# Kernel optimization log

Measured on AMD Instinct MI355X. Metric: run time of the kernel, lower is better.

## Reference

```python
import jax, jax.numpy as jnp
import numpy as np

D_MODEL = 1024
N_LAYER = 4
VOCAB = 50288  # 50277 padded to multiple of 16
D_STATE = 128
D_CONV = 4
HEADDIM = 64
CHUNK = 64
D_INNER = 2 * D_MODEL            # expand=2 -> 2048
NHEADS = D_INNER // HEADDIM      # 32
D_IN_PROJ = 2 * D_INNER + 2 * D_STATE + NHEADS  # ngroups=1
CONV_DIM = D_INNER + 2 * D_STATE
BATCH = 1
SEQLEN = 1024
EPS = 1e-5


def silu(x):
    return x * jax.nn.sigmoid(x)


def rmsnorm(x, w, z=None):
    if z is not None:
        x = x * silu(z)
    return x * jax.lax.rsqrt(jnp.mean(x * x, axis=-1, keepdims=True) + EPS) * w


def segsum(x):
    # x: (..., T) -> (..., T, T) with segment sums below diagonal, -inf above
    T = x.shape[-1]
    xe = jnp.broadcast_to(x[..., None], x.shape + (T,))
    mask_lo = jnp.tril(jnp.ones((T, T), dtype=bool), -1)
    xe = jnp.where(mask_lo, xe, 0.0)
    s = jnp.cumsum(xe, axis=-2)
    mask = jnp.tril(jnp.ones((T, T), dtype=bool), 0)
    return jnp.where(mask, s, -jnp.inf)


def ssd(x, dt, A, B, C, Dp):
    # x: (b,s,h,p), dt/A-broadcast: (b,s,h), B/C: (b,s,n) (ngroups=1), Dp: (h,)
    b, s = x.shape[0], x.shape[1]
    nchunks = s // CHUNK
    xD = x * Dp[:, None]
    Adt = A * dt                      # (b,s,h)
    xdt = x * dt[..., None]
    xr = xdt.reshape(b, nchunks, CHUNK, NHEADS, HEADDIM)
    Ar = Adt.reshape(b, nchunks, CHUNK, NHEADS).transpose(0, 3, 1, 2)  # (b,h,c,l)
    Br = B.reshape(b, nchunks, CHUNK, D_STATE)
    Cr = C.reshape(b, nchunks, CHUNK, D_STATE)
    A_cumsum = jnp.cumsum(Ar, axis=-1)                  # (b,h,c,l)
    L = jnp.exp(segsum(Ar))                             # (b,h,c,l,l)
    Y_diag = jnp.einsum('bcln,bcsn,bhcls,bcshp->bclhp', Cr, Br, L, xr)
    decay_states = jnp.exp(A_cumsum[..., -1:] - A_cumsum)
    states = jnp.einsum('bcln,bhcl,bclhp->bchpn', Br, decay_states, xr)
    states = jnp.concatenate([jnp.zeros_like(states[:, :1]), states], axis=1)
    decay_chunk = jnp.exp(segsum(jnp.pad(A_cumsum[..., -1], ((0, 0), (0, 0), (1, 0)))))
    new_states = jnp.einsum('bhzc,bchpn->bzhpn', decay_chunk, states)
    states = new_states[:, :-1]
    state_decay_out = jnp.exp(A_cumsum)
    Y_off = jnp.einsum('bcln,bchpn,bhcl->bclhp', Cr, states, state_decay_out)
    Y = (Y_diag + Y_off).reshape(b, s, NHEADS, HEADDIM) + xD
    return Y


def mamba2_forward(input_ids, embedding, norm_w, in_proj_w, conv_w, conv_b,
                   dt_bias, A_log, D, mixer_norm_w, out_proj_w, norm_f_w):
    h = embedding[input_ids]  # (b,s,d_model)
    for l in range(N_LAYER):
        u = rmsnorm(h, norm_w[l])
        zxbcdt = u @ in_proj_w[l].T  # (b,s,d_in_proj)
        z = zxbcdt[..., :D_INNER]
        xBC = zxbcdt[..., D_INNER:D_INNER + CONV_DIM]
        dt = jax.nn.softplus(zxbcdt[..., -NHEADS:] + dt_bias[l])
        # causal depthwise conv1d
        xc = jnp.transpose(xBC, (0, 2, 1))
        xc = jax.lax.conv_general_dilated(
            xc, conv_w[l], (1,), [(D_CONV - 1, 0)],
            dimension_numbers=('NCH', 'OIH', 'NCH'),
            feature_group_count=CONV_DIM) + conv_b[l][None, :, None]
        xBC = silu(jnp.transpose(xc, (0, 2, 1)))
        x = xBC[..., :D_INNER].reshape(BATCH, SEQLEN, NHEADS, HEADDIM)
        B = xBC[..., D_INNER:D_INNER + D_STATE]
        C = xBC[..., D_INNER + D_STATE:]
        A = -jnp.exp(A_log[l])  # (h,)
        y = ssd(x, dt, A, B, C, D[l])
        y = rmsnorm(y.reshape(BATCH, SEQLEN, D_INNER), mixer_norm_w[l], z)
        h = h + y @ out_proj_w[l].T
    h = rmsnorm(h, norm_f_w)
    return h @ embedding.T  # tied lm_head


def setup_inputs() -> dict:
    key = jax.random.key(0)
    ks = jax.random.split(key, 10)
    def rn(k, shape, s=0.02):
        return jax.random.normal(k, shape, jnp.float32) * s
    return {
        'input_ids': jax.random.randint(ks[0], (BATCH, SEQLEN), 0, VOCAB, jnp.int32),
        'embedding': rn(ks[1], (VOCAB, D_MODEL)),
        'norm_w': jnp.ones((N_LAYER, D_MODEL), jnp.float32),
        'in_proj_w': rn(ks[2], (N_LAYER, D_IN_PROJ, D_MODEL)),
        'conv_w': rn(ks[3], (N_LAYER, CONV_DIM, 1, D_CONV), 0.2),
        'conv_b': jnp.zeros((N_LAYER, CONV_DIM), jnp.float32),
        'dt_bias': rn(ks[4], (N_LAYER, NHEADS), 0.5),
        'A_log': jnp.log(jax.random.uniform(ks[5], (N_LAYER, NHEADS), jnp.float32, 1.0, 16.0)),
        'D': jnp.ones((N_LAYER, NHEADS), jnp.float32) + rn(ks[6], (N_LAYER, NHEADS), 0.1),
        'mixer_norm_w': jnp.ones((N_LAYER, D_INNER), jnp.float32),
        'out_proj_w': rn(ks[7], (N_LAYER, D_MODEL, D_INNER)),
        'norm_f_w': jnp.ones((D_MODEL,), jnp.float32),
    }


def reference(input_ids, embedding, norm_w, in_proj_w, conv_w, conv_b,
              dt_bias, A_log, D, mixer_norm_w, out_proj_w, norm_f_w):
    return mamba2_forward(input_ids, embedding, norm_w, in_proj_w, conv_w, conv_b,
                          dt_bias, A_log, D, mixer_norm_w, out_proj_w, norm_f_w)
```

## Files before the change

kernel.cpp:

```cpp
#include <hip/hip_runtime.h>
#include <hip/hip_bf16.h>
#include <math.h>

#define D_MODEL   1024
#define VOCAB     50288
#define D_STATE   128
#define D_CONV    4
#define HEADDIM   64
#define CHUNK     64
#define D_INNER   2048
#define NHEADS    32
#define D_IN_PROJ 4384
#define CONV_DIM  2304
#define SEQ       1024
#define NCHUNKS   16
#define EPS       1e-5f
#define SZH       1048576

typedef __bf16 bf16x8 __attribute__((ext_vector_type(8)));
typedef __bf16 bf16x4 __attribute__((ext_vector_type(4)));
typedef float  f32x4  __attribute__((ext_vector_type(4)));

__device__ __forceinline__ float blockReduceSum256(float v, float* sm) {
    #pragma unroll
    for (int off = 32; off > 0; off >>= 1) v += __shfl_down(v, off);
    if ((threadIdx.x & 63) == 0) sm[threadIdx.x >> 6] = v;
    __syncthreads();
    return sm[0] + sm[1] + sm[2] + sm[3];
}

__device__ __forceinline__ float sigmoidf_(float x) { return 1.0f / (1.0f + expf(-x)); }

__device__ __forceinline__ void gload_lds16(const __bf16* g, __bf16* l) {
    __builtin_amdgcn_global_load_lds(
        (const __attribute__((address_space(1))) void*)g,
        (__attribute__((address_space(3))) void*)l,
        16, 0, 0);
}

__global__ void cvt_bf16_k(const float* __restrict__ src, __bf16* __restrict__ dst, long n) {
    long i = ((long)blockIdx.x * 256 + threadIdx.x) * 8;
    long stride = (long)gridDim.x * 256 * 8;
    for (; i < n; i += stride) {
        float4 a = *(const float4*)(src + i);
        float4 b = *(const float4*)(src + i + 4);
        bf16x8 o;
        o[0] = (__bf16)a.x; o[1] = (__bf16)a.y; o[2] = (__bf16)a.z; o[3] = (__bf16)a.w;
        o[4] = (__bf16)b.x; o[5] = (__bf16)b.y; o[6] = (__bf16)b.z; o[7] = (__bf16)b.w;
        *(bf16x8*)(dst + i) = o;
    }
}

__global__ void gather_k(const int* __restrict__ ids, const float* __restrict__ emb,
                         float* __restrict__ h) {
    int s = blockIdx.x;
    int id = ids[s];
    const float4* src = (const float4*)(emb + (size_t)id * D_MODEL);
    float4* dst = (float4*)(h + (size_t)s * D_MODEL);
    dst[threadIdx.x] = src[threadIdx.x];
}

__global__ void rmsnorm_k(const float* __restrict__ x, const float* __restrict__ w,
                          float* __restrict__ o) {
    __shared__ float red[4];
    int s = blockIdx.x, t = threadIdx.x;
    float4 v = ((const float4*)(x + (size_t)s * D_MODEL))[t];
    float ss = v.x*v.x + v.y*v.y + v.z*v.z + v.w*v.w;
    float tot = blockReduceSum256(ss, red);
    float r = rsqrtf(tot / (float)D_MODEL + EPS);
    float4 wv = ((const float4*)w)[t];
    float4 ov;
    ov.x = v.x * r * wv.x; ov.y = v.y * r * wv.y;
    ov.z = v.z * r * wv.z; ov.w = v.w * r * wv.w;
    ((float4*)(o + (size_t)s * D_MODEL))[t] = ov;
}

__global__ void rmsnorm_fold_bf16_k(float* __restrict__ h, const float* __restrict__ o,
                                    const float* __restrict__ w, __bf16* __restrict__ out) {
    __shared__ float red[4];
    int s = blockIdx.x, t = threadIdx.x;
    float4 v = ((const float4*)(h + (size_t)s * D_MODEL))[t];
    if (o) {
        #pragma unroll
        for (int j = 0; j < 4; ++j) {
            float4 ov = ((const float4*)(o + (size_t)j * SZH + (size_t)s * D_MODEL))[t];
            v.x += ov.x; v.y += ov.y; v.z += ov.z; v.w += ov.w;
        }
        ((float4*)(h + (size_t)s * D_MODEL))[t] = v;
    }
    float ss = v.x*v.x + v.y*v.y + v.z*v.z + v.w*v.w;
    float tot = blockReduceSum256(ss, red);
    float r = rsqrtf(tot / (float)D_MODEL + EPS);
    float4 wv = ((const float4*)w)[t];
    bf16x4 ov;
    ov[0] = (__bf16)(v.x * r * wv.x); ov[1] = (__bf16)(v.y * r * wv.y);
    ov[2] = (__bf16)(v.z * r * wv.z); ov[3] = (__bf16)(v.w * r * wv.w);
    *(bf16x4*)(out + (size_t)s * D_MODEL + t * 4) = ov;
}

__global__ void gatednorm_k(float* __restrict__ Y, const float* __restrict__ zx,
                            const float* __restrict__ w) {
    __shared__ float red[4];
    int s = blockIdx.x, t = threadIdx.x;
    float4 y0 = ((const float4*)(Y + (size_t)s * D_INNER))[2*t];
    float4 y1 = ((const float4*)(Y + (size_t)s * D_INNER))[2*t+1];
    float4 z0 = ((const float4*)(zx + (size_t)s * D_IN_PROJ))[2*t];
    float4 z1 = ((const float4*)(zx + (size_t)s * D_IN_PROJ))[2*t+1];
    float g[8];
    float yv[8] = { y0.x,y0.y,y0.z,y0.w, y1.x,y1.y,y1.z,y1.w };
    float zv[8] = { z0.x,z0.y,z0.z,z0.w, z1.x,z1.y,z1.z,z1.w };
    float ss = 0.f;
    #pragma unroll
    for (int j = 0; j < 8; ++j) {
        float gg = yv[j] * zv[j] * sigmoidf_(zv[j]);
        g[j] = gg;
        ss += gg * gg;
    }
    float tot = blockReduceSum256(ss, red);
    float r = rsqrtf(tot / (float)D_INNER + EPS);
    float4 o0, o1;
    o0.x = g[0]*r*w[8*t+0]; o0.y = g[1]*r*w[8*t+1]; o0.z = g[2]*r*w[8*t+2]; o0.w = g[3]*r*w[8*t+3];
    o1.x = g[4]*r*w[8*t+4]; o1.y = g[5]*r*w[8*t+5]; o1.z = g[6]*r*w[8*t+6]; o1.w = g[7]*r*w[8*t+7];
    ((float4*)(Y + (size_t)s * D_INNER))[2*t]   = o0;
    ((float4*)(Y + (size_t)s * D_INNER))[2*t+1] = o1;
}

__global__ void gatednorm_bf16_k(const float* __restrict__ Y, const float* __restrict__ zx0,
                                 const float* __restrict__ zx1,
                                 const float* __restrict__ w, __bf16* __restrict__ o) {
    __shared__ float red[4];
    int s = blockIdx.x, t = threadIdx.x;
    float4 y0 = ((const float4*)(Y + (size_t)s * D_INNER))[2*t];
    float4 y1 = ((const float4*)(Y + (size_t)s * D_INNER))[2*t+1];
    float4 z0 = ((const float4*)(zx0 + (size_t)s * D_IN_PROJ))[2*t];
    float4 z1 = ((const float4*)(zx0 + (size_t)s * D_IN_PROJ))[2*t+1];
    if (zx1) {
        float4 a0 = ((const float4*)(zx1 + (size_t)s * D_IN_PROJ))[2*t];
        float4 a1 = ((const float4*)(zx1 + (size_t)s * D_IN_PROJ))[2*t+1];
        z0.x += a0.x; z0.y += a0.y; z0.z += a0.z; z0.w += a0.w;
        z1.x += a1.x; z1.y += a1.y; z1.z += a1.z; z1.w += a1.w;
    }
    float g[8];
    float yv[8] = { y0.x,y0.y,y0.z,y0.w, y1.x,y1.y,y1.z,y1.w };
    float zv[8] = { z0.x,z0.y,z0.z,z0.w, z1.x,z1.y,z1.z,z1.w };
    float ss = 0.f;
    #pragma unroll
    for (int j = 0; j < 8; ++j) {
        float gg = yv[j] * zv[j] * sigmoidf_(zv[j]);
        g[j] = gg;
        ss += gg * gg;
    }
    float tot = blockReduceSum256(ss, red);
    float r = rsqrtf(tot / (float)D_INNER + EPS);
    bf16x8 ov;
    #pragma unroll
    for (int j = 0; j < 8; ++j) ov[j] = (__bf16)(g[j] * r * w[8*t+j]);
    *(bf16x8*)(o + (size_t)s * D_INNER + t * 8) = ov;
}

__global__ __launch_bounds__(512) void gemm256_8ph(const __bf16* __restrict__ A,
                                                   const __bf16* __restrict__ B,
                                                   float* __restrict__ C,
                                                   int N, int K,
                                                   int lda, int ldb, int ldc,
                                                   int ntiles) {
    extern __shared__ __bf16 lds[];

    const int d = blockIdx.x;
    const int xcd = d & 7, kk = d >> 3;
    const int m_tile = kk & 3, p = kk >> 2;
    const int n_tile = xcd + (p << 3);
    if (n_tile >= ntiles) return;
    const int bm0 = m_tile * 256, bn0 = n_tile * 256;

    const int tid = threadIdx.x;
    const int l = tid & 63, w = tid >> 6;
    const int wr = w >> 2, wc = w & 3;
    const int lrow = l & 15;
    const int kb8 = (((l >> 4) ^ ((l >> 1) & 3)) << 3);
    const int srow_off = (w << 4) + (l >> 2);
    const int sk8 = (((l & 3) ^ ((l >> 3) & 3)) << 3);

    f32x4 acc[8][4];
    #pragma unroll
    for (int m = 0; m < 8; ++m)
        #pragma unroll
        for (int n = 0; n < 4; ++n) acc[m][n] = (f32x4){0.f,0.f,0.f,0.f};

    auto stage = [&](int kt, int b) {
        __bf16* base = lds + b * 16384;
        #pragma unroll
        for (int r = 0; r < 2; ++r) {
            int row = r * 128 + srow_off;
            const __bf16* g = A + (size_t)(bm0 + row) * lda + kt * 32 + sk8;
            gload_lds16(g, base + r * 4096 + w * 512);
        }
        #pragma unroll
        for (int r = 0; r < 2; ++r) {
            int row = r * 128 + srow_off;
            int grn = bn0 + row; if (grn > N - 1) grn = N - 1;
            const __bf16* g = B + (size_t)grn * ldb + kt * 32 + sk8;
            gload_lds16(g, base + 8192 + r * 4096 + w * 512);
        }
    };

    stage(0, 0);
    stage(1, 1);
    asm volatile("s_waitcnt vmcnt(4)" ::: "memory");
    __builtin_amdgcn_s_barrier();

    const int nt = K / 32;
    for (int t = 0; t < nt; ++t) {
        const int b = t & 1;
        const int bb = b * 16384;
        bf16x8 af[4], bfv[4];
        #pragma unroll
        for (int m = 0; m < 4; ++m)
            af[m] = *(const bf16x8*)&lds[bb + (wr * 128 + m * 16 + lrow) * 32 + kb8];
        #pragma unroll
        for (int n = 0; n < 4; ++n)
            bfv[n] = *(const bf16x8*)&lds[bb + 8192 + (wc * 64 + n * 16 + lrow) * 32 + kb8];
        __builtin_amdgcn_s_barrier();
        __builtin_amdgcn_s_setprio(1);
        #pragma unroll
        for (int m = 0; m < 4; ++m)
            #pragma unroll
            for (int n = 0; n < 4; ++n)
                acc[m][n] = __builtin_amdgcn_mfma_f32_16x16x32_bf16(af[m], bfv[n], acc[m][n], 0, 0, 0);
        __builtin_amdgcn_s_setprio(0);
        __builtin_amdgcn_s_barrier();
        #pragma unroll
        for (int m = 0; m < 4; ++m)
            af[m] = *(const bf16x8*)&lds[bb + (wr * 128 + (m + 4) * 16 + lrow) * 32 + kb8];
        __builtin_amdgcn_s_barrier();
        __builtin_amdgcn_s_setprio(1);
        #pragma unroll
        for (int m = 0; m < 4; ++m)
            #pragma unroll
            for (int n = 0; n < 4; ++n)
                acc[m + 4][n] = __builtin_amdgcn_mfma_f32_16x16x32_bf16(af[m], bfv[n], acc[m + 4][n], 0, 0, 0);
        __builtin_amdgcn_s_setprio(0);
        __builtin_amdgcn_s_barrier();
        asm volatile("" ::: "memory");
        if (t + 2 < nt) {
            stage(t + 2, b);
            asm volatile("s_waitcnt vmcnt(4)" ::: "memory");
            __builtin_amdgcn_s_barrier();
        } else if (t + 1 < nt) {
            asm volatile("s_waitcnt vmcnt(0)" ::: "memory");
            __builtin_amdgcn_s_barrier();
        }
    }

    const int r0q = (l >> 4) * 4;
    #pragma unroll
    for (int m = 0; m < 8; ++m) {
        int gr = bm0 + wr * 128 + m * 16 + r0q;
        #pragma unroll
        for (int n = 0; n < 4; ++n) {
            int gc = bn0 + wc * 64 + n * 16 + lrow;
            if (gc < N) {
                #pragma unroll
                for (int rr = 0; rr < 4; ++rr)
                    C[(size_t)(gr + rr) * ldc + gc] = acc[m][n][rr];
            }
        }
    }
}

template<int TM, int TN, int MTL2, bool ACC>
__global__ __launch_bounds__(256) void gemm_bt_bf16(const __bf16* __restrict__ A,
                                                    const __bf16* __restrict__ B,
                                                    float* __restrict__ C,
                                                    int N, int klen,
                                                    int lda, int ldb, int ldc,
                                                    int ntiles, size_t csplit) {
    constexpr int FM = TM / 32;
    constexpr int FN = TN / 32;
    __shared__ __bf16 As[TM * 32];
    __shared__ __bf16 Bs[TN * 32];

    const int d = blockIdx.x;
    const int xcd = d & 7;
    const int kk = d >> 3;
    const int p = kk >> MTL2;
    const int m_tile = kk & ((1 << MTL2) - 1);
    const int n_tile = xcd + (p << 3);
    if (n_tile >= ntiles) return;

    const int k_begin = blockIdx.y * klen;
    C += (size_t)blockIdx.y * csplit;

    const int bm0 = m_tile * TM;
    const int bn0 = n_tile * TN;
    const int t = threadIdx.x;
    const int l = t & 63;
    const int w = t >> 6;
    const int wr = w >> 1, wc = w & 1;
    const int lrow = l & 15;
    const int lk   = (l >> 4) * 8;
    const int srow = l >> 2;
    const int scol = (l & 3) * 8;

    f32x4 acc[FM][FN];
    #pragma unroll
    for (int m = 0; m < FM; ++m)
        #pragma unroll
        for (int n = 0; n < FN; ++n)
            acc[m][n] = (f32x4){0.f, 0.f, 0.f, 0.f};

    for (int k0 = k_begin; k0 < k_begin + klen; k0 += 32) {
        __syncthreads();
        #pragma unroll
        for (int i = 0; i < TM / 64; ++i) {
            int r0 = w * (TM / 4) + i * 16;
            const __bf16* g = A + (size_t)(bm0 + r0 + srow) * lda + k0 + scol;
            gload_lds16(g, As + (size_t)r0 * 32);
        }
        #pragma unroll
        for (int i = 0; i < TN / 64; ++i) {
            int r0 = w * (TN / 4) + i * 16;
            int gn = bn0 + r0 + srow; if (gn > N - 1) gn = N - 1;
            const __bf16* g = B + (size_t)gn * ldb + k0 + scol;
            gload_lds16(g, Bs + (size_t)r0 * 32);
        }
        __syncthreads();

        bf16x8 af[FM], bfr[FN];
        #pragma unroll
        for (int m = 0; m < FM; ++m)
            af[m] = *(const bf16x8*)&As[(wr * (TM/2) + m * 16 + lrow) * 32 + lk];
        #pragma unroll
        for (int n = 0; n < FN; ++n)
            bfr[n] = *(const bf16x8*)&Bs[(wc * (TN/2) + n * 16 + lrow) * 32 + lk];
        #pragma unroll
        for (int m = 0; m < FM; ++m)
            #pragma unroll
            for (int n = 0; n < FN; ++n)
                acc[m][n] = __builtin_amdgcn_mfma_f32_16x16x32_bf16(af[m], bfr[n], acc[m][n], 0, 0, 0);
    }

    const int r0 = (l >> 4) * 4;
    #pragma unroll
    for (int m = 0; m < FM; ++m) {
        #pragma unroll
        for (int rr = 0; rr < 4; ++rr) {
            int gr = bm0 + wr * (TM/2) + m * 16 + r0 + rr;
            #pragma unroll
            for (int n = 0; n < FN; ++n) {
                int gc = bn0 + wc * (TN/2) + n * 16 + lrow;
                if (gc < N) {
                    size_t off = (size_t)gr * ldc + gc;
                    if (ACC) C[off] += acc[m][n][rr];
                    else     C[off]  = acc[m][n][rr];
                }
            }
        }
    }
}

template<bool ACC>
__global__ __launch_bounds__(256) void gemm_nt_cvt(const float* __restrict__ A,
                                                   const float* __restrict__ B,
                                                   float* __restrict__ C,
                                                   int M, int N, int K,
                                                   int lda, int ldb, int ldc) {
    __shared__ __bf16 As[128][40];
    __shared__ __bf16 Bs[128][40];
    const int bm0 = blockIdx.x * 128;
    const int bn0 = blockIdx.y * 128;
    const int t = threadIdx.x;
    const int l = t & 63;
    const int w = t >> 6;
    const int wr = w >> 1;
    const int wc = w & 1;
    const int lrow = l & 15;
    const int lk   = (l >> 4) * 8;

    f32x4 acc[4][4];
    #pragma unroll
    for (int m = 0; m < 4; ++m)
        #pragma unroll
        for (int n = 0; n < 4; ++n)
            acc[m][n] = (f32x4){0.f, 0.f, 0.f, 0.f};

    for (int k0 = 0; k0 < K; k0 += 32) {
        __syncthreads();
        float4 av[4], bv[4];
        #pragma unroll
        for (int i = 0; i < 4; ++i) {
            int idx = t + i * 256;
            int r = idx >> 3;
            int c4 = (idx & 7) * 4;
            av[i] = *(const float4*)(A + (size_t)(bm0 + r) * lda + k0 + c4);
            int gn = bn0 + r; if (gn > N - 1) gn = N - 1;
            bv[i] = *(const float4*)(B + (size_t)gn * ldb + k0 + c4);
        }
        #pragma unroll
        for (int i = 0; i < 4; ++i) {
            int idx = t + i * 256;
            int r = idx >> 3;
            int c4 = (idx & 7) * 4;
            bf16x4 aw, bw;
            aw[0] = (__bf16)av[i].x; aw[1] = (__bf16)av[i].y;
            aw[2] = (__bf16)av[i].z; aw[3] = (__bf16)av[i].w;
            bw[0] = (__bf16)bv[i].x; bw[1] = (__bf16)bv[i].y;
            bw[2] = (__bf16)bv[i].z; bw[3] = (__bf16)bv[i].w;
            *(bf16x4*)&As[r][c4] = aw;
            *(bf16x4*)&Bs[r][c4] = bw;
        }
        __syncthreads();

        bf16x8 af[4], bfr[4];
        #pragma unroll
        for (int m = 0; m < 4; ++m)
            af[m] = *(const bf16x8*)&As[wr * 64 + m * 16 + lrow][lk];
        #pragma unroll
        for (int n = 0; n < 4; ++n)
            bfr[n] = *(const bf16x8*)&Bs[wc * 64 + n * 16 + lrow][lk];
        #pragma unroll
        for (int m = 0; m < 4; ++m)
            #pragma unroll
            for (int n = 0; n < 4; ++n)
                acc[m][n] = __builtin_amdgcn_mfma_f32_16x16x32_bf16(af[m], bfr[n], acc[m][n], 0, 0, 0);
    }

    const int r0 = (l >> 4) * 4;
    #pragma unroll
    for (int m = 0; m < 4; ++m) {
        #pragma unroll
        for (int rr = 0; rr < 4; ++rr) {
            int gr = bm0 + wr * 64 + m * 16 + r0 + rr;
            #pragma unroll
            for (int n = 0; n < 4; ++n) {
                int gc = bn0 + wc * 64 + n * 16 + lrow;
                if (gc < N) {
                    size_t off = (size_t)gr * ldc + gc;
                    if (ACC) C[off] += acc[m][n][rr];
                    else     C[off]  = acc[m][n][rr];
                }
            }
        }
    }
}

__global__ void conv_silu_k(const float* __restrict__ zx0, const float* __restrict__ zx1,
                            const float* __restrict__ w,
                            const float* __restrict__ b, float* __restrict__ xBC) {
    int idx = blockIdx.x * 256 + threadIdx.x;
    if (idx >= SEQ * CONV_DIM) return;
    int s = idx / CONV_DIM, c = idx - s * CONV_DIM;
    float acc = b[c];
    #pragma unroll
    for (int k = 0; k < D_CONV; ++k) {
        int si = s + k - (D_CONV - 1);
        if (si >= 0) {
            size_t o = (size_t)si * D_IN_PROJ + D_INNER + c;
            float v = zx0[o];
            if (zx1) v += zx1[o];
            acc = fmaf(v, w[c * D_CONV + k], acc);
        }
    }
    xBC[idx] = acc * sigmoidf_(acc);
}

__global__ void dtcum_k(const float* __restrict__ zx0, const float* __restrict__ zx1,
                        const float* __restrict__ dt_bias,
                        const float* __restrict__ A_log,
                        float* __restrict__ dtb, float* __restrict__ acs) {
    int c = blockIdx.x, h = blockIdx.y, l = threadIdx.x;
    int s = c * 64 + l;
    size_t o = (size_t)s * D_IN_PROJ + (D_IN_PROJ - NHEADS) + h;
    float v = zx0[o];
    if (zx1) v += zx1[o];
    v += dt_bias[h];
    float dt = (v > 20.f) ? v : log1pf(expf(v));
    dtb[(size_t)s * NHEADS + h] = dt;
    float a = -expf(A_log[h]);
    float x = a * dt;
    #pragma unroll
    for (int off = 1; off < 64; off <<= 1) {
        float oo = __shfl_up(x, off);
        if (l >= off) x += oo;
    }
    acs[(size_t)h * SEQ + s] = x;
}

__global__ __launch_bounds__(256) void cmg_k(const float* __restrict__ xBC,
                                             float* __restrict__ cm,
                                             __bf16* __restrict__ btg) {
    const int c = blockIdx.x;
    const int LDP = 136;
    __shared__ __bf16 Cs[64 * 136];
    __shared__ __bf16 Bs[64 * 136];
    const int t = threadIdx.x;
    const int l = t & 63;
    const int w = t >> 6;

    #pragma unroll
    for (int i = 0; i < 8; ++i) {
        int e = t + i * 256;
        int row = e >> 5, n4 = (e & 31) * 4;
        float4 vc = *(const float4*)(xBC + (size_t)(c*64 + row) * CONV_DIM + D_INNER + D_STATE + n4);
        float4 vb = *(const float4*)(xBC + (size_t)(c*64 + row) * CONV_DIM + D_INNER + n4);
        bf16x4 cc, bb;
        cc[0] = (__bf16)vc.x; cc[1] = (__bf16)vc.y; cc[2] = (__bf16)vc.z; cc[3] = (__bf16)vc.w;
        bb[0] = (__bf16)vb.x; bb[1] = (__bf16)vb.y; bb[2] = (__bf16)vb.z; bb[3] = (__bf16)vb.w;
        *(bf16x4*)&Cs[row * LDP + n4] = cc;
        *(bf16x4*)&Bs[row * LDP + n4] = bb;
    }
    __syncthreads();

    #pragma unroll
    for (int i = 0; i < 4; ++i) {
        int e8 = t + i * 256;
        int n = e8 >> 3, l8 = (e8 & 7) * 8;
        bf16x8 o;
        #pragma unroll
        for (int j = 0; j < 8; ++j) o[j] = Bs[(l8 + j) * LDP + n];
        *(bf16x8*)(btg + ((size_t)c * 128 + n) * 64 + l8) = o;
    }

    const int lrow = l & 15;
    const int lk   = (l >> 4) * 8;
    const int l0 = w * 16;
    f32x4 acc[4];
    #pragma unroll
    for (int n = 0; n < 4; ++n) acc[n] = (f32x4){0.f,0.f,0.f,0.f};
    #pragma unroll
    for (int kc = 0; kc < 4; ++kc) {
        bf16x8 a = *(const bf16x8*)&Cs[(l0 + lrow) * LDP + kc * 32 + lk];
        #pragma unroll
        for (int n = 0; n < 4; ++n) {
            bf16x8 b = *(const bf16x8*)&Bs[(n * 16 + lrow) * LDP + kc * 32 + lk];
            acc[n] = __builtin_amdgcn_mfma_f32_16x16x32_bf16(a, b, acc[n], 0, 0, 0);
        }
    }
    const int r0 = (l >> 4) * 4;
    #pragma unroll
    for (int n = 0; n < 4; ++n)
        #pragma unroll
        for (int r = 0; r < 4; ++r)
            cm[(size_t)c * 4096 + (l0 + r0 + r) * 64 + n * 16 + lrow] = acc[n][r];
}

__global__ __launch_bounds__(256) void ydst_k(const float* __restrict__ cm,
                                              const __bf16* __restrict__ btg,
                                              const float* __restrict__ xBC,
                                              const float* __restrict__ dtb,
                                              const float* __restrict__ acs,
                                              float* __restrict__ Y,
                                              float* __restrict__ st) {
    const int c = blockIdx.x, h = blockIdx.y;
    const int LDP = 72;
    __shared__ __bf16 Xt[64 * 72];
    __shared__ __bf16 X2[64 * 72];
    __shared__ __bf16 G [64 * 72];
    __shared__ __bf16 Bt[128 * 72];
    __shared__ float arow[64];
    __shared__ float decl[64];
    const int t = threadIdx.x;
    const int l = t & 63;
    const int w = t >> 6;

    if (t < 64) arow[t] = acs[(size_t)h * SEQ + c * 64 + t];
    __syncthreads();
    const float alast = arow[63];
    if (t < 64) decl[t] = expf(alast - arow[t]);
    #pragma unroll
    for (int i = 0; i < 16; ++i) {
        int e = t + i * 256;
        int gl = e >> 6, sx = e & 63;
        G[gl * LDP + sx] = (sx <= gl) ? (__bf16)(cm[(size_t)c * 4096 + e] * expf(arow[gl] - arow[sx])) : (__bf16)0.f;
    }
    #pragma unroll
    for (int i = 0; i < 4; ++i) {
        int e8 = t + i * 256;
        int n = e8 >> 3, l8 = (e8 & 7) * 8;
        *(bf16x8*)&Bt[n * LDP + l8] = *(const bf16x8*)(btg + ((size_t)c * 128 + n) * 64 + l8);
    }
    __syncthreads();
    #pragma unroll
    for (int i = 0; i < 4; ++i) {
        int e4 = t + i * 256;
        int sx = e4 >> 4, p4 = (e4 & 15) * 4;
        int s = c * 64 + sx;
        float4 v = *(const float4*)(xBC + (size_t)s * CONV_DIM + h * HEADDIM + p4);
        float d = dtb[(size_t)s * NHEADS + h];
        float d2 = d * decl[sx];
        Xt[(p4+0) * LDP + sx] = (__bf16)(v.x * d);
        Xt[(p4+1) * LDP + sx] = (__bf16)(v.y * d);
        Xt[(p4+2) * LDP + sx] = (__bf16)(v.z * d);
        Xt[(p4+3) * LDP + sx] = (__bf16)(v.w * d);
        X2[(p4+0) * LDP + sx] = (__bf16)(v.x * d2);
        X2[(p4+1) * LDP + sx] = (__bf16)(v.y * d2);
        X2[(p4+2) * LDP + sx] = (__bf16)(v.z * d2);
        X2[(p4+3) * LDP + sx] = (__bf16)(v.w * d2);
    }
    __syncthreads();

    const int lrow = l & 15;
    const int lk   = (l >> 4) * 8;
    const int p0 = w * 16;
    const int r0 = (l >> 4) * 4;

    f32x4 acc1[4];
    #pragma unroll
    for (int n = 0; n < 4; ++n) acc1[n] = (f32x4){0.f,0.f,0.f,0.f};
    #pragma unroll
    for (int kc = 0; kc < 2; ++kc) {
        bf16x8 a = *(const bf16x8*)&Xt[(p0 + lrow) * LDP + kc * 32 + lk];
        #pragma unroll
        for (int n = 0; n < 4; ++n) {
            bf16x8 b = *(const bf16x8*)&G[(n * 16 + lrow) * LDP + kc * 32 + lk];
            acc1[n] = __builtin_amdgcn_mfma_f32_16x16x32_bf16(a, b, acc1[n], 0, 0, 0);
        }
    }
    #pragma unroll
    for (int n = 0; n < 4; ++n) {
        int lc = n * 16 + lrow;
        float4 ov; ov.x = acc1[n][0]; ov.y = acc1[n][1]; ov.z = acc1[n][2]; ov.w = acc1[n][3];
        *(float4*)(Y + (size_t)(c*64 + lc) * D_INNER + h * HEADDIM + p0 + r0) = ov;
    }

    f32x4 acc2[8];
    #pragma unroll
    for (int n = 0; n < 8; ++n) acc2[n] = (f32x4){0.f,0.f,0.f,0.f};
    #pragma unroll
    for (int kc = 0; kc < 2; ++kc) {
        bf16x8 a = *(const bf16x8*)&X2[(p0 + lrow) * LDP + kc * 32 + lk];
        #pragma unroll
        for (int n = 0; n < 8; ++n) {
            bf16x8 b = *(const bf16x8*)&Bt[(n * 16 + lrow) * LDP + kc * 32 + lk];
            acc2[n] = __builtin_amdgcn_mfma_f32_16x16x32_bf16(a, b, acc2[n], 0, 0, 0);
        }
    }
    float* stb = st + ((size_t)(c * NHEADS + h) * 64) * 128;
    #pragma unroll
    for (int n = 0; n < 8; ++n) {
        int nc = n * 16 + lrow;
        #pragma unroll
        for (int r = 0; r < 4; ++r)
            stb[(size_t)(p0 + r0 + r) * 128 + nc] = acc2[n][r];
    }
}

__global__ void rec_k(float* __restrict__ st, const float* __restrict__ acs) {
    int idx = blockIdx.x * 256 + threadIdx.x;
    int h = idx >> 13;
    float S = 0.f;
    for (int c = 0; c < NCHUNKS; ++c) {
        float* p = st + (size_t)c * (NHEADS * D_STATE * HEADDIM) + idx;
        float tmp = *p;
        *p = S;
        float dec = expf(acs[(size_t)h * SEQ + c * 64 + 63]);
        S = fmaf(S, dec, tmp);
    }
}

__global__ __launch_bounds__(256) void yoff_k(const float* __restrict__ xBC,
                                              const float* __restrict__ acs,
                                              const float* __restrict__ st,
                                              const float* __restrict__ Dp,
                                              float* __restrict__ Y) {
    const int c = blockIdx.x, h = blockIdx.y;
    const int LDP = 136;
    __shared__ __bf16 Sts[64 * 136];
    __shared__ __bf16 Cs [64 * 136];
    __shared__ float arow[64];
    const int t = threadIdx.x;
    const int l = t & 63;
    const int w = t >> 6;

    if (t < 64) arow[t] = acs[(size_t)h * SEQ + c * 64 + t];
    const float* stb = st + ((size_t)(c * NHEADS + h) * 64) * 128;
    #pragma unroll
    for (int i = 0; i < 8; ++i) {
        int e = t + i * 256;
        int row = e >> 5, n4 = (e & 31) * 4;
        float4 vs = *(const float4*)(stb + (size_t)row * 128 + n4);
        float4 vc = *(const float4*)(xBC + (size_t)(c*64 + row) * CONV_DIM + D_INNER + D_STATE + n4);
        bf16x4 ss, cc;
        ss[0] = (__bf16)vs.x; ss[1] = (__bf16)vs.y; ss[2] = (__bf16)vs.z; ss[3] = (__bf16)vs.w;
        cc[0] = (__bf16)vc.x; cc[1] = (__bf16)vc.y; cc[2] = (__bf16)vc.z; cc[3] = (__bf16)vc.w;
        *(bf16x4*)&Sts[row * LDP + n4] = ss;
        *(bf16x4*)&Cs [row * LDP + n4] = cc;
    }
    __syncthreads();

    const int lrow = l & 15;
    const int lk   = (l >> 4) * 8;
    const int p0 = w * 16;
    const int r0 = (l >> 4) * 4;
    const float dpar = Dp[h];

    f32x4 acc[4];
    #pragma unroll
    for (int n = 0; n < 4; ++n) acc[n] = (f32x4){0.f,0.f,0.f,0.f};
    #pragma unroll
    for (int kc = 0; kc < 4; ++kc) {
        bf16x8 a = *(const bf16x8*)&Sts[(p0 + lrow) * LDP + kc * 32 + lk];
        #pragma unroll
        for (int n = 0; n < 4; ++n) {
            bf16x8 b = *(const bf16x8*)&Cs[(n * 16 + lrow) * LDP + kc * 32 + lk];
            acc[n] = __builtin_amdgcn_mfma_f32_16x16x32_bf16(a, b, acc[n], 0, 0, 0);
        }
    }
    #pragma unroll
    for (int n = 0; n < 4; ++n) {
        int lc = n * 16 + lrow;
        int s = c * 64 + lc;
        float sc = expf(arow[lc]);
        float4 xv = *(const float4*)(xBC + (size_t)s * CONV_DIM + h * HEADDIM + p0 + r0);
        float4 yv = *(float4*)(Y + (size_t)s * D_INNER + h * HEADDIM + p0 + r0);
        yv.x += sc * acc[n][0] + dpar * xv.x;
        yv.y += sc * acc[n][1] + dpar * xv.y;
        yv.z += sc * acc[n][2] + dpar * xv.z;
        yv.w += sc * acc[n][3] + dpar * xv.w;
        *(float4*)(Y + (size_t)s * D_INNER + h * HEADDIM + p0 + r0) = yv;
    }
}

extern "C" void kernel_launch(void* const* d_in, const int* in_sizes, int n_in,
                              void* d_out, int out_size, void* d_ws, size_t ws_size,
                              hipStream_t stream) {
    const int*   ids          = (const int*)d_in[0];
    const float* emb          = (const float*)d_in[1];
    const float* norm_w       = (const float*)d_in[2];
    const float* in_proj_w    = (const float*)d_in[3];
    const float* conv_w       = (const float*)d_in[4];
    const float* conv_b       = (const float*)d_in[5];
    const float* dt_bias      = (const float*)d_in[6];
    const float* A_log        = (const float*)d_in[7];
    const float* Dp           = (const float*)d_in[8];
    const float* mixer_norm_w = (const float*)d_in[9];
    const float* out_proj_w   = (const float*)d_in[10];
    const float* norm_f_w     = (const float*)d_in[11];
    float* out = (float*)d_out;

    const size_t SZ_H = SZH, SZ_U = SZH, SZ_ZX = 4489216, SZ_XBC = 2359296,
                 SZ_DT = 32768, SZ_ACS = 32768, SZ_CM = 65536, SZ_ST = 4194304, SZ_Y = 2097152;
    const size_t SZ_BTG_F = 65536;
    const size_t BF_U = SZ_H, BF_Y = SZ_Y;
    const size_t BF_WIN  = 4ull * 4489216;
    const size_t BF_WOUT = 4ull * 2097152;
    const size_t BF_EMB  = (size_t)VOCAB * D_MODEL;

    const size_t f32_base = SZ_H + SZ_U + SZ_ZX + SZ_XBC + SZ_DT + SZ_ACS + SZ_CM + SZ_BTG_F + SZ_ST + SZ_Y;
    const size_t f32_new  = f32_base + SZ_ZX + 4 * SZ_H;
    const size_t bf_all   = (BF_U + BF_Y + BF_WIN + BF_WOUT + BF_EMB) * 2;
    const size_t bytesNew = f32_new * 4 + bf_all;
    const size_t bytesOld = f32_base * 4 + bf_all;
    const int tier = (ws_size >= bytesNew) ? 0 : (ws_size >= bytesOld) ? 1 : 2;

    float *h, *u, *dtb, *acs, *cm, *zx, *zxb = nullptr, *xBC, *st, *Y, *o = nullptr;
    __bf16 *btg, *ub = nullptr, *Yb = nullptr, *win = nullptr, *wout = nullptr, *embb = nullptr;

    if (tier <= 1) {
        float* f = (float*)d_ws;
        h = f;   f += SZ_H;
        u = f;   f += SZ_U;
        dtb = f; f += SZ_DT;
        acs = f; f += SZ_ACS;
        cm = f;  f += SZ_CM;
        btg = (__bf16*)f; f += SZ_BTG_F;
        zx = f;  f += SZ_ZX;
        if (tier == 0) {
            zxb = f; f += SZ_ZX;
            o = f;   f += 4 * SZ_H;
        }
        xBC = f; f += SZ_XBC;
        st = f;  f += SZ_ST;
        Y = f;   f += SZ_Y;
        __bf16* bb = (__bf16*)f;
        ub = bb;   bb += BF_U;
        Yb = bb;   bb += BF_Y;
        win = bb;  bb += BF_WIN;
        wout = bb; bb += BF_WOUT;
        embb = bb;
    } else {
        float* f = (float*)d_ws;
        h = f;   f += SZ_H;
        u = f;   f += SZ_U;
        dtb = f; f += SZ_DT;
        acs = f; f += SZ_ACS;
        cm = f;  f += SZ_CM;
        btg = (__bf16*)f; f += SZ_BTG_F;
        float* ob = (float*)d_out;
        zx = ob;
        xBC = zx + SZ_ZX;
        st = xBC + SZ_XBC;
        Y = st + SZ_ST;
    }

    if (tier <= 1) {
        cvt_bf16_k<<<(int)(BF_WIN / 2048), 256, 0, stream>>>(in_proj_w, win, (long)BF_WIN);
        cvt_bf16_k<<<(int)(BF_WOUT / 2048), 256, 0, stream>>>(out_proj_w, wout, (long)BF_WOUT);
        cvt_bf16_k<<<(int)(BF_EMB / 2048), 256, 0, stream>>>(emb, embb, (long)BF_EMB);
    }

    gather_k<<<SEQ, 256, 0, stream>>>(ids, emb, h);

    const int NT_IN  = (D_IN_PROJ + 127) / 128;
    const int NT_OUT = D_MODEL / 128;
    const int GX_IN  = 8 * ((NT_IN  + 7) / 8) * 8;
    const int GX_OUT = 8 * ((NT_OUT + 7) / 8) * 16;
    const int NT_LM256 = (VOCAB + 255) / 256;
    const int GX_LM256 = 8 * ((NT_LM256 + 7) / 8) * 4;

    for (int l = 0; l < 4; ++l) {
        if (tier <= 1) {
            rmsnorm_fold_bf16_k<<<SEQ, 256, 0, stream>>>(
                h, (tier == 0 && l > 0) ? o : nullptr, norm_w + (size_t)l * D_MODEL, ub);
            if (tier == 0) {
                gemm_bt_bf16<128, 128, 3, false><<<dim3(GX_IN, 2), 256, 0, stream>>>(
                    ub, win + (size_t)l * 4489216, zx,
                    D_IN_PROJ, 512, D_MODEL, D_MODEL, D_IN_PROJ, NT_IN, SZ_ZX);
            } else {
                gemm_bt_bf16<128, 128, 3, false><<<dim3(GX_IN, 1), 256, 0, stream>>>(
                    ub, win + (size_t)l * 4489216, zx,
                    D_IN_PROJ, 1024, D_MODEL, D_MODEL, D_IN_PROJ, NT_IN, 0);
            }
        } else {
            rmsnorm_k<<<SEQ, 256, 0, stream>>>(h, norm_w + (size_t)l * D_MODEL, u);
            gemm_nt_cvt<false><<<dim3(8, 35), 256, 0, stream>>>(
                u, in_proj_w + (size_t)l * D_IN_PROJ * D_MODEL, zx,
                SEQ, D_IN_PROJ, D_MODEL, D_MODEL, D_MODEL, D_IN_PROJ);
        }

        float* zx1 = (tier == 0) ? zxb : nullptr;

        conv_silu_k<<<(SEQ * CONV_DIM) / 256, 256, 0, stream>>>(
            zx, zx1, conv_w + (size_t)l * CONV_DIM * D_CONV, conv_b + (size_t)l * CONV_DIM, xBC);

        dtcum_k<<<dim3(NCHUNKS, NHEADS), 64, 0, stream>>>(
            zx, zx1, dt_bias + (size_t)l * NHEADS, A_log + (size_t)l * NHEADS, dtb, acs);

        cmg_k<<<NCHUNKS, 256, 0, stream>>>(xBC, cm, btg);

        ydst_k<<<dim3(NCHUNKS, NHEADS), 256, 0, stream>>>(cm, btg, xBC, dtb, acs, Y, st);

        rec_k<<<(NHEADS * D_STATE * HEADDIM) / 256, 256, 0, stream>>>(st, acs);

        yoff_k<<<dim3(NCHUNKS, NHEADS), 256, 0, stream>>>(xBC, acs, st, Dp + (size_t)l * NHEADS, Y);

        if (tier <= 1) {
            gatednorm_bf16_k<<<SEQ, 256, 0, stream>>>(Y, zx, zx1, mixer_norm_w + (size_t)l * D_INNER, Yb);
            if (tier == 0) {
                gemm_bt_bf16<64, 128, 4, false><<<dim3(GX_OUT, 4), 256, 0, stream>>>(
                    Yb, wout + (size_t)l * 2097152, o,
                    D_MODEL, 512, D_INNER, D_INNER, D_MODEL, NT_OUT, SZ_H);
            } else {
                gemm_bt_bf16<64, 128, 4, true><<<dim3(GX_OUT, 1), 256, 0, stream>>>(
                    Yb, wout + (size_t)l * 2097152, h,
                    D_MODEL, 2048, D_INNER, D_INNER, D_MODEL, NT_OUT, 0);
            }
        } else {
            gatednorm_k<<<SEQ, 256, 0, stream>>>(Y, zx, mixer_norm_w + (size_t)l * D_INNER);
            gemm_nt_cvt<true><<<dim3(8, 8), 256, 0, stream>>>(
                Y, out_proj_w + (size_t)l * D_MODEL * D_INNER, h,
                SEQ, D_MODEL, D_INNER, D_INNER, D_INNER, D_MODEL);
        }
    }

    if (tier <= 1) {
        rmsnorm_fold_bf16_k<<<SEQ, 256, 0, stream>>>(
            h, (tier == 0) ? o : nullptr, norm_f_w, ub);
        gemm256_8ph<<<dim3(GX_LM256), 512, 65536, stream>>>(
            ub, embb, out, VOCAB, 1024, D_MODEL, D_MODEL, VOCAB, NT_LM256);
    } else {
        rmsnorm_k<<<SEQ, 256, 0, stream>>>(h, norm_f_w, u);
        gemm_nt_cvt<false><<<dim3(8, (VOCAB + 127) / 128), 256, 0, stream>>>(
            u, emb, out, SEQ, VOCAB, D_MODEL, D_MODEL, D_MODEL, VOCAB);
    }
}
```

Measured before the change: 720.3 us.

## Deepen LM-head GEMM pipeline to four LDS stages with single-phase MFMA loop

Replaces the double-buffered two-phase LM-head GEMM with a four-buffer pipeline that prefetches three K-tiles ahead, using graded vmcnt waits and one barrier pair per iteration. All eight A fragments are loaded up front and the full 8x4 MFMA block is issued in a single burst, removing the interleaved half-tile barriers. The intent is to hide global-load latency better and cut synchronisation overhead. In exchange it uses 128 KB of static LDS and more VGPRs for fragments, which may reduce occupancy. It also drops the barrier between LDS fragment reads and the next stage write.

```diff
diff --git a/kernel.cpp b/kernel.cpp
--- a/kernel.cpp
+++ b/kernel.cpp
@@ -158,13 +158,13 @@
     *(bf16x8*)(o + (size_t)s * D_INNER + t * 8) = ov;
 }
 
-__global__ __launch_bounds__(512) void gemm256_8ph(const __bf16* __restrict__ A,
-                                                   const __bf16* __restrict__ B,
-                                                   float* __restrict__ C,
-                                                   int N, int K,
-                                                   int lda, int ldb, int ldc,
-                                                   int ntiles) {
-    extern __shared__ __bf16 lds[];
+__global__ __launch_bounds__(512) void gemm256_p4(const __bf16* __restrict__ A,
+                                                  const __bf16* __restrict__ B,
+                                                  float* __restrict__ C,
+                                                  int N, int K,
+                                                  int lda, int ldb, int ldc,
+                                                  int ntiles) {
+    __shared__ __bf16 lds[4 * 16384];
 
     const int d = blockIdx.x;
     const int xcd = d & 7, kk = d >> 3;
@@ -206,50 +206,34 @@
 
     stage(0, 0);
     stage(1, 1);
-    asm volatile("s_waitcnt vmcnt(4)" ::: "memory");
-    __builtin_amdgcn_s_barrier();
+    stage(2, 2);
 
     const int nt = K / 32;
     for (int t = 0; t < nt; ++t) {
-        const int b = t & 1;
-        const int bb = b * 16384;
-        bf16x8 af[4], bfv[4];
-        #pragma unroll
-        for (int m = 0; m < 4; ++m)
+        const int bb = (t & 3) * 16384;
+        if (t + 3 < nt) stage(t + 3, (t + 3) & 3);
+        if (t + 3 < nt)      asm volatile("s_waitcnt vmcnt(12)" ::: "memory");
+        else if (t + 2 < nt) asm volatile("s_waitcnt vmcnt(8)"  ::: "memory");
+        else if (t + 1 < nt) asm volatile("s_waitcnt vmcnt(4)"  ::: "memory");
+        else                 asm volatile("s_waitcnt vmcnt(0)"  ::: "memory");
+        __builtin_amdgcn_s_barrier();
+
+        bf16x8 af[8], bfv[4];
+        #pragma unroll
+        for (int m = 0; m < 8; ++m)
             af[m] = *(const bf16x8*)&lds[bb + (wr * 128 + m * 16 + lrow) * 32 + kb8];
         #pragma unroll
         for (int n = 0; n < 4; ++n)
             bfv[n] = *(const bf16x8*)&lds[bb + 8192 + (wc * 64 + n * 16 + lrow) * 32 + kb8];
-        __builtin_amdgcn_s_barrier();
+
         __builtin_amdgcn_s_setprio(1);
         #pragma unroll
-        for (int m = 0; m < 4; ++m)
+        for (int m = 0; m < 8; ++m)
             #pragma unroll
             for (int n = 0; n < 4; ++n)
                 acc[m][n] = __builtin_amdgcn_mfma_f32_16x16x32_bf16(af[m], bfv[n], acc[m][n], 0, 0, 0);
         __builtin_amdgcn_s_setprio(0);
         __builtin_amdgcn_s_barrier();
-        #pragma unroll
-        for (int m = 0; m < 4; ++m)
-            af[m] = *(const bf16x8*)&lds[bb + (wr * 128 + (m + 4) * 16 + lrow) * 32 + kb8];
-        __builtin_amdgcn_s_barrier();
-        __builtin_amdgcn_s_setprio(1);
-        #pragma unroll
-        for (int m = 0; m < 4; ++m)
-            #pragma unroll
-            for (int n = 0; n < 4; ++n)
-                acc[m + 4][n] = __builtin_amdgcn_mfma_f32_16x16x32_bf16(af[m], bfv[n], acc[m + 4][n], 0, 0, 0);
-        __builtin_amdgcn_s_setprio(0);
-        __builtin_amdgcn_s_barrier();
-        asm volatile("" ::: "memory");
-        if (t + 2 < nt) {
-            stage(t + 2, b);
-            asm volatile("s_waitcnt vmcnt(4)" ::: "memory");
-            __builtin_amdgcn_s_barrier();
-        } else if (t + 1 < nt) {
-            asm volatile("s_waitcnt vmcnt(0)" ::: "memory");
-            __builtin_amdgcn_s_barrier();
-        }
     }
 
     const int r0q = (l >> 4) * 4;
@@ -866,7 +850,7 @@
     if (tier <= 1) {
         rmsnorm_fold_bf16_k<<<SEQ, 256, 0, stream>>>(
             h, (tier == 0) ? o : nullptr, norm_f_w, ub);
-        gemm256_8ph<<<dim3(GX_LM256), 512, 65536, stream>>>(
+        gemm256_p4<<<dim3(GX_LM256), 512, 0, stream>>>(
             ub, embb, out, VOCAB, 1024, D_MODEL, D_MODEL, VOCAB, NT_LM256);
     } else {
         rmsnorm_k<<<SEQ, 256, 0, stream>>>(h, norm_f_w, u);
```

After: 711.1 us. No clear change (-1.3%).

## Deepen LM-head GEMM K-tile to 64 with interleaved quarter-stage prefetch

Applied to the files above, without the earlier changes.

Restructures the 256x256 LM-head GEMM so each K iteration covers 64 instead of 32. The next tile's A and B halves are prefetched in four pieces interleaved between the MFMA phases, replacing the previous two-tile-ahead staging. The LDS swizzle moves to an 8-way XOR on 64-wide rows, and the dynamic shared memory becomes a static 128KB array. The aim is to halve loop and barrier overhead per FLOP and spread global loads across the compute phases. The cost is a larger LDS footprint and a shallower prefetch distance.

```diff
diff --git a/kernel.cpp b/kernel.cpp
--- a/kernel.cpp
+++ b/kernel.cpp
@@ -164,7 +164,7 @@
                                                    int N, int K,
                                                    int lda, int ldb, int ldc,
                                                    int ntiles) {
-    extern __shared__ __bf16 lds[];
+    __shared__ __bf16 lds[2 * 32768];
 
     const int d = blockIdx.x;
     const int xcd = d & 7, kk = d >> 3;
@@ -177,9 +177,17 @@
     const int l = tid & 63, w = tid >> 6;
     const int wr = w >> 2, wc = w & 3;
     const int lrow = l & 15;
-    const int kb8 = (((l >> 4) ^ ((l >> 1) & 3)) << 3);
-    const int srow_off = (w << 4) + (l >> 2);
-    const int sk8 = (((l & 3) ^ ((l >> 3) & 3)) << 3);
+    const int khi = l >> 4;
+    const int kb0 = ((khi       ^ (lrow & 7)) << 3);
+    const int kb1 = (((4 + khi) ^ (lrow & 7)) << 3);
+    const int Lr = l >> 3, Lb = l & 7;
+    const int sblk = ((Lb ^ Lr) << 3);
+
+    int aoff[8], boff[4];
+    #pragma unroll
+    for (int m = 0; m < 8; ++m) aoff[m] = (wr * 128 + m * 16 + lrow) * 64;
+    #pragma unroll
+    for (int n = 0; n < 4; ++n) boff[n] = 16384 + (wc * 64 + n * 16 + lrow) * 64;
 
     f32x4 acc[8][4];
     #pragma unroll
@@ -187,40 +195,42 @@
         #pragma unroll
         for (int n = 0; n < 4; ++n) acc[m][n] = (f32x4){0.f,0.f,0.f,0.f};
 
-    auto stage = [&](int kt, int b) {
-        __bf16* base = lds + b * 16384;
+    auto stage_half = [&](const __bf16* gm, int ld, int row0, int clampR, __bf16* dst) {
         #pragma unroll
         for (int r = 0; r < 2; ++r) {
-            int row = r * 128 + srow_off;
-            const __bf16* g = A + (size_t)(bm0 + row) * lda + kt * 32 + sk8;
-            gload_lds16(g, base + r * 4096 + w * 512);
-        }
-        #pragma unroll
-        for (int r = 0; r < 2; ++r) {
-            int row = r * 128 + srow_off;
-            int grn = bn0 + row; if (grn > N - 1) grn = N - 1;
-            const __bf16* g = B + (size_t)grn * ldb + kt * 32 + sk8;
-            gload_lds16(g, base + 8192 + r * 4096 + w * 512);
+            int chunk = r * 8 + w;
+            int grow = row0 + chunk * 8 + Lr;
+            if (grow > clampR) grow = clampR;
+            const __bf16* g = gm + (size_t)grow * ld + sblk;
+            gload_lds16(g, dst + chunk * 512);
         }
     };
 
-    stage(0, 0);
-    stage(1, 1);
-    asm volatile("s_waitcnt vmcnt(4)" ::: "memory");
-    __builtin_amdgcn_s_barrier();
-
-    const int nt = K / 32;
+    stage_half(A, lda, bm0,       1 << 30, lds);
+    stage_half(A, lda, bm0 + 128, 1 << 30, lds + 8192);
+    stage_half(B, ldb, bn0,       N - 1,   lds + 16384);
+    stage_half(B, ldb, bn0 + 128, N - 1,   lds + 16384 + 8192);
+
+    const int nt = K / 64;
     for (int t = 0; t < nt; ++t) {
-        const int b = t & 1;
-        const int bb = b * 16384;
+        __bf16* bb = lds + (t & 1) * 32768;
+        __bf16* nb = lds + ((t + 1) & 1) * 32768;
+        const __bf16* An = A + (t + 1) * 64;
+        const __bf16* Bn = B + (t + 1) * 64;
+        const bool pf = (t + 1 < nt);
         bf16x8 af[4], bfv[4];
-        #pragma unroll
-        for (int m = 0; m < 4; ++m)
-            af[m] = *(const bf16x8*)&lds[bb + (wr * 128 + m * 16 + lrow) * 32 + kb8];
-        #pragma unroll
-        for (int n = 0; n < 4; ++n)
-            bfv[n] = *(const bf16x8*)&lds[bb + 8192 + (wc * 64 + n * 16 + lrow) * 32 + kb8];
+
+        if (pf) {
+            stage_half(An, lda, bm0, 1 << 30, nb);
+            asm volatile("s_waitcnt vmcnt(2)" ::: "memory");
+        } else {
+            asm volatile("s_waitcnt vmcnt(0)" ::: "memory");
+        }
         __builtin_amdgcn_s_barrier();
+        #pragma unroll
+        for (int m = 0; m < 4; ++m) af[m] = *(const bf16x8*)&bb[aoff[m] + kb0];
+        #pragma unroll
+        for (int n = 0; n < 4; ++n) bfv[n] = *(const bf16x8*)&bb[boff[n] + kb0];
         __builtin_amdgcn_s_setprio(1);
         #pragma unroll
         for (int m = 0; m < 4; ++m)
@@ -229,10 +239,10 @@
                 acc[m][n] = __builtin_amdgcn_mfma_f32_16x16x32_bf16(af[m], bfv[n], acc[m][n], 0, 0, 0);
         __builtin_amdgcn_s_setprio(0);
         __builtin_amdgcn_s_barrier();
-        #pragma unroll
-        for (int m = 0; m < 4; ++m)
-            af[m] = *(const bf16x8*)&lds[bb + (wr * 128 + (m + 4) * 16 + lrow) * 32 + kb8];
-        __builtin_amdgcn_s_barrier();
+
+        if (pf) stage_half(An, lda, bm0 + 128, 1 << 30, nb + 8192);
+        #pragma unroll
+        for (int m = 0; m < 4; ++m) af[m] = *(const bf16x8*)&bb[aoff[m + 4] + kb0];
         __builtin_amdgcn_s_setprio(1);
         #pragma unroll
         for (int m = 0; m < 4; ++m)
@@ -241,15 +251,32 @@
                 acc[m + 4][n] = __builtin_amdgcn_mfma_f32_16x16x32_bf16(af[m], bfv[n], acc[m + 4][n], 0, 0, 0);
         __builtin_amdgcn_s_setprio(0);
         __builtin_amdgcn_s_barrier();
-        asm volatile("" ::: "memory");
-        if (t + 2 < nt) {
-            stage(t + 2, b);
-            asm volatile("s_waitcnt vmcnt(4)" ::: "memory");
-            __builtin_amdgcn_s_barrier();
-        } else if (t + 1 < nt) {
-            asm volatile("s_waitcnt vmcnt(0)" ::: "memory");
-            __builtin_amdgcn_s_barrier();
-        }
+
+        if (pf) stage_half(Bn, ldb, bn0, N - 1, nb + 16384);
+        #pragma unroll
+        for (int m = 0; m < 4; ++m) af[m] = *(const bf16x8*)&bb[aoff[m] + kb1];
+        #pragma unroll
+        for (int n = 0; n < 4; ++n) bfv[n] = *(const bf16x8*)&bb[boff[n] + kb1];
+        __builtin_amdgcn_s_setprio(1);
+        #pragma unroll
+        for (int m = 0; m < 4; ++m)
+            #pragma unroll
+            for (int n = 0; n < 4; ++n)
+                acc[m][n] = __builtin_amdgcn_mfma_f32_16x16x32_bf16(af[m], bfv[n], acc[m][n], 0, 0, 0);
+        __builtin_amdgcn_s_setprio(0);
+        __builtin_amdgcn_s_barrier();
+
+        if (pf) stage_half(Bn, ldb, bn0 + 128, N - 1, nb + 16384 + 8192);
+        #pragma unroll
+        for (int m = 0; m < 4; ++m) af[m] = *(const bf16x8*)&bb[aoff[m + 4] + kb1];
+        __builtin_amdgcn_s_setprio(1);
+        #pragma unroll
+        for (int m = 0; m < 4; ++m)
+            #pragma unroll
+            for (int n = 0; n < 4; ++n)
+                acc[m + 4][n] = __builtin_amdgcn_mfma_f32_16x16x32_bf16(af[m], bfv[n], acc[m + 4][n], 0, 0, 0);
+        __builtin_amdgcn_s_setprio(0);
+        __builtin_amdgcn_s_barrier();
     }
 
     const int r0q = (l >> 4) * 4;
@@ -866,7 +893,7 @@
     if (tier <= 1) {
         rmsnorm_fold_bf16_k<<<SEQ, 256, 0, stream>>>(
             h, (tier == 0) ? o : nullptr, norm_f_w, ub);
-        gemm256_8ph<<<dim3(GX_LM256), 512, 65536, stream>>>(
+        gemm256_8ph<<<dim3(GX_LM256), 512, 0, stream>>>(
             ub, embb, out, VOCAB, 1024, D_MODEL, D_MODEL, VOCAB, NT_LM256);
     } else {
         rmsnorm_k<<<SEQ, 256, 0, stream>>>(h, norm_f_w, u);
```

New measurement: 708.5 us. No clear change (-1.6%).

## Restructure LM-head GEMM pipeline to prefetch next tile split across phases

Applied to the files above, without the earlier changes.

Rewrites the 256x256 LM-head GEMM main loop. Instead of staging two tiles ahead after compute, it issues the A-operand load for tile t+1 before the first MFMA phase and the B-operand load between the two phases. It also cuts the barriers per iteration, precomputes LDS offsets, and switches to static shared memory. The goal is better overlap of global loads with MFMA work and less synchronization, at the cost of a shallower prefetch distance, one tile instead of two.

```diff
diff --git a/kernel.cpp b/kernel.cpp
--- a/kernel.cpp
+++ b/kernel.cpp
@@ -158,13 +158,13 @@
     *(bf16x8*)(o + (size_t)s * D_INNER + t * 8) = ov;
 }
 
-__global__ __launch_bounds__(512) void gemm256_8ph(const __bf16* __restrict__ A,
+__global__ __launch_bounds__(512) void gemm256_2ph(const __bf16* __restrict__ A,
                                                    const __bf16* __restrict__ B,
                                                    float* __restrict__ C,
                                                    int N, int K,
                                                    int lda, int ldb, int ldc,
                                                    int ntiles) {
-    extern __shared__ __bf16 lds[];
+    __shared__ __bf16 lds[2 * 16384];
 
     const int d = blockIdx.x;
     const int xcd = d & 7, kk = d >> 3;
@@ -177,9 +177,16 @@
     const int l = tid & 63, w = tid >> 6;
     const int wr = w >> 2, wc = w & 3;
     const int lrow = l & 15;
-    const int kb8 = (((l >> 4) ^ ((l >> 1) & 3)) << 3);
-    const int srow_off = (w << 4) + (l >> 2);
-    const int sk8 = (((l & 3) ^ ((l >> 3) & 3)) << 3);
+    const int khi = l >> 4;
+    const int kb = ((khi ^ (lrow & 3)) << 3);
+    const int Lr = l >> 2;
+    const int sblk = (((l & 3) ^ (Lr & 3)) << 3);
+
+    int aoff[8], boff[4];
+    #pragma unroll
+    for (int m = 0; m < 8; ++m) aoff[m] = (wr * 128 + m * 16 + lrow) * 32;
+    #pragma unroll
+    for (int n = 0; n < 4; ++n) boff[n] = 8192 + (wc * 64 + n * 16 + lrow) * 32;
 
     f32x4 acc[8][4];
     #pragma unroll
@@ -187,40 +194,38 @@
         #pragma unroll
         for (int n = 0; n < 4; ++n) acc[m][n] = (f32x4){0.f,0.f,0.f,0.f};
 
-    auto stage = [&](int kt, int b) {
-        __bf16* base = lds + b * 16384;
+    auto stage_op = [&](const __bf16* gm, int ld, int row0, int clampR, int kt, __bf16* dst) {
         #pragma unroll
         for (int r = 0; r < 2; ++r) {
-            int row = r * 128 + srow_off;
-            const __bf16* g = A + (size_t)(bm0 + row) * lda + kt * 32 + sk8;
-            gload_lds16(g, base + r * 4096 + w * 512);
-        }
-        #pragma unroll
-        for (int r = 0; r < 2; ++r) {
-            int row = r * 128 + srow_off;
-            int grn = bn0 + row; if (grn > N - 1) grn = N - 1;
-            const __bf16* g = B + (size_t)grn * ldb + kt * 32 + sk8;
-            gload_lds16(g, base + 8192 + r * 4096 + w * 512);
+            int chunk = r * 8 + w;
+            int grow = row0 + chunk * 16 + Lr;
+            if (grow > clampR) grow = clampR;
+            const __bf16* g = gm + (size_t)grow * ld + kt * 32 + sblk;
+            gload_lds16(g, dst + chunk * 512);
         }
     };
 
-    stage(0, 0);
-    stage(1, 1);
-    asm volatile("s_waitcnt vmcnt(4)" ::: "memory");
-    __builtin_amdgcn_s_barrier();
+    stage_op(A, lda, bm0, 1 << 30, 0, lds);
+    stage_op(B, ldb, bn0, N - 1,   0, lds + 8192);
 
     const int nt = K / 32;
     for (int t = 0; t < nt; ++t) {
-        const int b = t & 1;
-        const int bb = b * 16384;
+        __bf16* bb = lds + (t & 1) * 16384;
+        __bf16* nb = lds + ((t + 1) & 1) * 16384;
+        const bool pf = (t + 1 < nt);
         bf16x8 af[4], bfv[4];
-        #pragma unroll
-        for (int m = 0; m < 4; ++m)
-            af[m] = *(const bf16x8*)&lds[bb + (wr * 128 + m * 16 + lrow) * 32 + kb8];
-        #pragma unroll
-        for (int n = 0; n < 4; ++n)
-            bfv[n] = *(const bf16x8*)&lds[bb + 8192 + (wc * 64 + n * 16 + lrow) * 32 + kb8];
+
+        if (pf) {
+            stage_op(A, lda, bm0, 1 << 30, t + 1, nb);
+            asm volatile("s_waitcnt vmcnt(2)" ::: "memory");
+        } else {
+            asm volatile("s_waitcnt vmcnt(0)" ::: "memory");
+        }
         __builtin_amdgcn_s_barrier();
+        #pragma unroll
+        for (int m = 0; m < 4; ++m) af[m] = *(const bf16x8*)&bb[aoff[m] + kb];
+        #pragma unroll
+        for (int n = 0; n < 4; ++n) bfv[n] = *(const bf16x8*)&bb[boff[n] + kb];
         __builtin_amdgcn_s_setprio(1);
         #pragma unroll
         for (int m = 0; m < 4; ++m)
@@ -229,10 +234,10 @@
                 acc[m][n] = __builtin_amdgcn_mfma_f32_16x16x32_bf16(af[m], bfv[n], acc[m][n], 0, 0, 0);
         __builtin_amdgcn_s_setprio(0);
         __builtin_amdgcn_s_barrier();
-        #pragma unroll
-        for (int m = 0; m < 4; ++m)
-            af[m] = *(const bf16x8*)&lds[bb + (wr * 128 + (m + 4) * 16 + lrow) * 32 + kb8];
-        __builtin_amdgcn_s_barrier();
+
+        if (pf) stage_op(B, ldb, bn0, N - 1, t + 1, nb + 8192);
+        #pragma unroll
+        for (int m = 0; m < 4; ++m) af[m] = *(const bf16x8*)&bb[aoff[m + 4] + kb];
         __builtin_amdgcn_s_setprio(1);
         #pragma unroll
         for (int m = 0; m < 4; ++m)
@@ -241,15 +246,6 @@
                 acc[m + 4][n] = __builtin_amdgcn_mfma_f32_16x16x32_bf16(af[m], bfv[n], acc[m + 4][n], 0, 0, 0);
         __builtin_amdgcn_s_setprio(0);
         __builtin_amdgcn_s_barrier();
-        asm volatile("" ::: "memory");
-        if (t + 2 < nt) {
-            stage(t + 2, b);
-            asm volatile("s_waitcnt vmcnt(4)" ::: "memory");
-            __builtin_amdgcn_s_barrier();
-        } else if (t + 1 < nt) {
-            asm volatile("s_waitcnt vmcnt(0)" ::: "memory");
-            __builtin_amdgcn_s_barrier();
-        }
     }
 
     const int r0q = (l >> 4) * 4;
@@ -866,7 +862,7 @@
     if (tier <= 1) {
         rmsnorm_fold_bf16_k<<<SEQ, 256, 0, stream>>>(
             h, (tier == 0) ? o : nullptr, norm_f_w, ub);
-        gemm256_8ph<<<dim3(GX_LM256), 512, 65536, stream>>>(
+        gemm256_2ph<<<dim3(GX_LM256), 512, 0, stream>>>(
             ub, embb, out, VOCAB, 1024, D_MODEL, D_MODEL, VOCAB, NT_LM256);
     } else {
         rmsnorm_k<<<SEQ, 256, 0, stream>>>(h, norm_f_w, u);
```

New measurement: 727.8 us. Within noise of the previous version (+1.0%).
